# Optimization experiments

Measured on AMD Instinct MI355X. Metric: run time of the kernel, lower is better.

## Reference

```python
import jax, jax.numpy as jnp
import numpy as np

B, SEQ, F = 256, 2048, 5
IN1, U1, U2 = SEQ * F, 32, 1
UNFOLDS = 6          # ODE solver unfolds per cell call
ELAPSED = 1.0        # elapsed time per call


def _cell_params(key, n_in, n_u):
    ks = jax.random.split(key, 9)
    U = lambda k, shp, lo, hi: jax.random.uniform(k, shp, jnp.float32, lo, hi)
    return dict(
        input_w=jnp.ones((n_in,), jnp.float32),
        input_b=jnp.zeros((n_in,), jnp.float32),
        smu=U(ks[0], (n_in, n_u), 0.3, 0.8),
        ssig=U(ks[1], (n_in, n_u), 3.0, 8.0),
        sW=U(ks[2], (n_in, n_u), 0.001, 1.0),
        serev=2.0 * jax.random.bernoulli(ks[3], 0.5, (n_in, n_u)).astype(jnp.float32) - 1.0,
        mu=U(ks[4], (n_u, n_u), 0.3, 0.8),
        sig=U(ks[5], (n_u, n_u), 3.0, 8.0),
        W=U(ks[6], (n_u, n_u), 0.001, 1.0),
        erev=2.0 * jax.random.bernoulli(ks[7], 0.5, (n_u, n_u)).astype(jnp.float32) - 1.0,
        gleak=jnp.ones((n_u,), jnp.float32),
        vleak=U(ks[8], (n_u,), -0.2, 0.2),
        cm=0.5 * jnp.ones((n_u,), jnp.float32),
    )


def setup_inputs() -> dict:
    key = jax.random.key(0)
    kx, ka, kb = jax.random.split(key, 3)
    inp = {"x": jax.random.normal(kx, (B, SEQ, F), jnp.float32)}
    for pfx, k, n_in, n_u in (("a_", ka, IN1, U1), ("b_", kb, U1, U2)):
        for name, v in _cell_params(k, n_in, n_u).items():
            inp[pfx + name] = v
    return inp


def _ltc(x, iw, ib, smu, ssig, sW, serev, mu, sig, W, erev, gleak, vleak, cm):
    # x: [B, n_in]; input affine mapping
    x = x * iw + ib
    # sensory synapse activations: [B, n_in, n_u]
    sact = sW * jax.nn.sigmoid((x[:, :, None] - smu) * ssig)
    w_num_s = jnp.einsum('biu,iu->bu', sact, serev)   # reversal-weighted sum
    w_den_s = jnp.sum(sact, axis=1)
    cm_t = cm / (ELAPSED / UNFOLDS)                   # [n_u]
    v0 = jnp.zeros((x.shape[0], cm.shape[0]), x.dtype)

    def body(v, _):
        # recurrent synapses: presyn axis 1, postsyn axis 2 -> [B, n_u, n_u]
        wact = W * jax.nn.sigmoid((v[:, :, None] - mu) * sig)
        num = cm_t * v + gleak * vleak + jnp.einsum('bij,ij->bj', wact, erev) + w_num_s
        den = cm_t + gleak + jnp.sum(wact, axis=1) + w_den_s
        return num / den, None

    v, _ = jax.lax.scan(body, v0, None, length=UNFOLDS)
    return v


def reference(x,
              a_input_w, a_input_b, a_smu, a_ssig, a_sW, a_serev,
              a_mu, a_sig, a_W, a_erev, a_gleak, a_vleak, a_cm,
              b_input_w, b_input_b, b_smu, b_ssig, b_sW, b_serev,
              b_mu, b_sig, b_W, b_erev, b_gleak, b_vleak, b_cm):
    bsz = x.shape[0]
    xb = x.reshape(bsz, -1)  # [B, seq*5]
    h = _ltc(xb, a_input_w, a_input_b, a_smu, a_ssig, a_sW, a_serev,
             a_mu, a_sig, a_W, a_erev, a_gleak, a_vleak, a_cm)     # [B, 32]
    h2 = _ltc(h, b_input_w, b_input_b, b_smu, b_ssig, b_sW, b_serev,
              b_mu, b_sig, b_W, b_erev, b_gleak, b_vleak, b_cm)    # [B, 1]
    return jax.nn.sigmoid(h2).reshape(bsz)
```

## Files before the change

kernel.cpp:

```cpp
#include <hip/hip_runtime.h>

#define BATCH 256
#define IN1   10240
#define NU    32
#define NB    32
#define BGROUPS (BATCH / NB)
#define CHUNK 40
#define XPAD  44
#define LOG2E 1.4426950408889634f

__global__ __launch_bounds__(256) void ltc_sensory_partial(
    const float* __restrict__ x,
    const float* __restrict__ iw, const float* __restrict__ ibias,
    const float* __restrict__ smu, const float* __restrict__ ssig,
    const float* __restrict__ sW, const float* __restrict__ serev,
    float2* __restrict__ part, int stripe)
{
    const int tid = threadIdx.x;
    const int u   = tid & 31;
    const int g   = tid >> 5;
    const int b0  = blockIdx.x * NB;
    const int ibase = blockIdx.y * stripe;
    const int iend  = ibase + stripe;

    __shared__ float4 sP[CHUNK * NU];
    __shared__ float  xL[NB][XPAD];

    float accn[4], accd[4];
#pragma unroll
    for (int k = 0; k < 4; ++k) { accn[k] = 0.f; accd[k] = 0.f; }

    const int lrow = tid >> 3;
    const int lq   = tid & 7;

    for (int cb = ibase; cb < iend; cb += CHUNK) {
        __syncthreads();

#pragma unroll
        for (int p = tid; p < CHUNK * NU; p += 256) {
            const int ii = cb + (p >> 5);
            const int gi = ii * NU + (p & 31);
            const float sg = ssig[gi] * LOG2E;
            const float w  = sW[gi];
            sP[p] = make_float4(sg * iw[ii],
                                (smu[gi] - ibias[ii]) * sg,
                                w, w * serev[gi]);
        }
        const float* xrow = x + (size_t)(b0 + lrow) * IN1 + cb;
        {
            const float4 v4 = *(const float4*)(xrow + lq * 4);
            *(float4*)&xL[lrow][lq * 4] = v4;
            if (lq < 2) {
                const float4 w4 = *(const float4*)(xrow + (lq + 8) * 4);
                *(float4*)&xL[lrow][(lq + 8) * 4] = w4;
            }
        }
        __syncthreads();

        const float* xr = &xL[g * 4][0];
#pragma unroll 2
        for (int di = 0; di < CHUNK; ++di) {
            const float4 f = sP[di * NU + u];
#pragma unroll
            for (int k = 0; k < 4; ++k) {
                const float xv = xr[k * XPAD + di];
                const float e  = __builtin_amdgcn_exp2f(f.y - xv * f.x);
                const float r  = __builtin_amdgcn_rcpf(1.0f + e);
                accd[k] = fmaf(f.z, r, accd[k]);
                accn[k] = fmaf(f.w, r, accn[k]);
            }
        }
    }

#pragma unroll
    for (int k = 0; k < 4; ++k) {
        part[((size_t)blockIdx.y * BATCH + (b0 + g * 4 + k)) * NU + u] =
            make_float2(accn[k], accd[k]);
    }
}

__global__ __launch_bounds__(256) void ltc_reduce(
    const float2* __restrict__ part, int nsplit, float2* __restrict__ S)
{
    const int tid = threadIdx.x;
    const int b   = blockIdx.x;
    const int u   = tid & 31;
    const int sl  = tid >> 5;

    __shared__ float sred[8][NU][2];

    float sn = 0.f, sd = 0.f;
#pragma unroll 8
    for (int s = sl; s < nsplit; s += 8) {
        const float2 p = part[((size_t)s * BATCH + b) * NU + u];
        sn += p.x;
        sd += p.y;
    }
    sred[sl][u][0] = sn;
    sred[sl][u][1] = sd;
    __syncthreads();

    if (tid >= 32) return;
    float Sn = 0.f, Sd = 0.f;
#pragma unroll
    for (int s2 = 0; s2 < 8; ++s2) {
        Sn += sred[s2][u][0];
        Sd += sred[s2][u][1];
    }
    S[(size_t)b * NU + u] = make_float2(Sn, Sd);
}

__global__ __launch_bounds__(256) void ltc_unfold(
    const float2* __restrict__ S,
    const float* __restrict__ amu, const float* __restrict__ asig,
    const float* __restrict__ aW,  const float* __restrict__ aerev,
    const float* __restrict__ agleak, const float* __restrict__ avleak,
    const float* __restrict__ acm,
    const float* __restrict__ b_iw, const float* __restrict__ b_ib,
    const float* __restrict__ b_smu, const float* __restrict__ b_ssig,
    const float* __restrict__ b_sW,  const float* __restrict__ b_serev,
    const float* __restrict__ b_mu,  const float* __restrict__ b_sig,
    const float* __restrict__ b_W,   const float* __restrict__ b_erev,
    const float* __restrict__ b_gleak, const float* __restrict__ b_vleak,
    const float* __restrict__ b_cm,
    float* __restrict__ out)
{
    const int tid = threadIdx.x;
    const int u   = tid & 31;
    const int bl  = tid >> 5;
    const int b   = blockIdx.x * 8 + bl;

    __shared__ float pAp[NU*NU], pCp[NU*NU];
    __shared__ float pW[NU*NU],  pWE[NU*NU];

    for (int p = tid; p < NU * NU; p += 256) {
        const float sg = asig[p] * LOG2E;
        pAp[p] = sg;
        pCp[p] = amu[p] * sg;
        const float w = aW[p];
        pW[p]  = w;
        pWE[p] = w * aerev[p];
    }
    __syncthreads();

    const float2 Sv = S[(size_t)b * NU + u];
    const float Sn = Sv.x, Sd = Sv.y;

    const float cmt = acm[u] * 6.0f;
    const float gl  = agleak[u];
    const float gv  = gl * avleak[u];

    float v = 0.f;
    for (int k = 0; k < 6; ++k) {
        float rn = 0.f, rd = 0.f;
#pragma unroll
        for (int j = 0; j < NU; ++j) {
            const float vj = __shfl(v, j, 32);
            const int pi = j * NU + u;
            const float e = __builtin_amdgcn_exp2f(pCp[pi] - vj * pAp[pi]);
            const float r = __builtin_amdgcn_rcpf(1.0f + e);
            rn = fmaf(pWE[pi], r, rn);
            rd = fmaf(pW[pi],  r, rd);
        }
        const float num = cmt * v + gv + rn + Sn;
        const float den = cmt + gl + rd + Sd;
        v = num / den;
    }

    const float x2  = v * b_iw[u] + b_ib[u];
    const float e2  = __builtin_amdgcn_exp2f((b_smu[u] - x2) * b_ssig[u] * LOG2E);
    const float s2v = b_sW[u] * __builtin_amdgcn_rcpf(1.0f + e2);
    float wn = s2v * b_serev[u];
    float wd = s2v;
#pragma unroll
    for (int m = 16; m >= 1; m >>= 1) {
        wn += __shfl_xor(wn, m, 32);
        wd += __shfl_xor(wd, m, 32);
    }

    const float bcmt = b_cm[0] * 6.0f;
    const float bgl  = b_gleak[0];
    const float bgv  = bgl * b_vleak[0];
    const float bmu  = b_mu[0], bsig = b_sig[0], bW = b_W[0], berev = b_erev[0];
    float v2 = 0.f;
#pragma unroll
    for (int k = 0; k < 6; ++k) {
        const float ee = __builtin_amdgcn_exp2f((bmu - v2) * bsig * LOG2E);
        const float ws = bW * __builtin_amdgcn_rcpf(1.0f + ee);
        const float num = bcmt * v2 + bgv + ws * berev + wn;
        const float den = bcmt + bgl + ws + wd;
        v2 = num / den;
    }

    if (u == 0)
        out[b] = 1.0f / (1.0f + __builtin_amdgcn_exp2f(-v2 * LOG2E));
}

extern "C" void kernel_launch(void* const* d_in, const int* in_sizes, int n_in,
                              void* d_out, int out_size, void* d_ws, size_t ws_size,
                              hipStream_t stream) {
    const float* x       = (const float*)d_in[0];
    const float* a_iw    = (const float*)d_in[1];
    const float* a_ib    = (const float*)d_in[2];
    const float* a_smu   = (const float*)d_in[3];
    const float* a_ssig  = (const float*)d_in[4];
    const float* a_sW    = (const float*)d_in[5];
    const float* a_serev = (const float*)d_in[6];
    const float* a_mu    = (const float*)d_in[7];
    const float* a_sig   = (const float*)d_in[8];
    const float* a_W     = (const float*)d_in[9];
    const float* a_erev  = (const float*)d_in[10];
    const float* a_gleak = (const float*)d_in[11];
    const float* a_vleak = (const float*)d_in[12];
    const float* a_cm    = (const float*)d_in[13];
    const float* b_iw    = (const float*)d_in[14];
    const float* b_ib    = (const float*)d_in[15];
    const float* b_smu   = (const float*)d_in[16];
    const float* b_ssig  = (const float*)d_in[17];
    const float* b_sW    = (const float*)d_in[18];
    const float* b_serev = (const float*)d_in[19];
    const float* b_mu    = (const float*)d_in[20];
    const float* b_sig   = (const float*)d_in[21];
    const float* b_W     = (const float*)d_in[22];
    const float* b_erev  = (const float*)d_in[23];
    const float* b_gleak = (const float*)d_in[24];
    const float* b_vleak = (const float*)d_in[25];
    const float* b_cm    = (const float*)d_in[26];
    float* out = (float*)d_out;

    int splits = 256;
    while (splits > 4 &&
           ((size_t)splits * BATCH * NU + BATCH * NU) * sizeof(float2) > ws_size)
        splits >>= 1;
    const int stripe = IN1 / splits;

    float2* part = (float2*)d_ws;
    float2* S    = part + (size_t)splits * BATCH * NU;

    dim3 grid1(BGROUPS, splits);
    ltc_sensory_partial<<<grid1, 256, 0, stream>>>(
        x, a_iw, a_ib, a_smu, a_ssig, a_sW, a_serev, part, stripe);

    ltc_reduce<<<BATCH, 256, 0, stream>>>(part, splits, S);

    ltc_unfold<<<BATCH / 8, 256, 0, stream>>>(
        S,
        a_mu, a_sig, a_W, a_erev, a_gleak, a_vleak, a_cm,
        b_iw, b_ib, b_smu, b_ssig, b_sW, b_serev,
        b_mu, b_sig, b_W, b_erev, b_gleak, b_vleak, b_cm,
        out);
}
```

Before: 45.08 us.

## Prepack sensory parameters and map batch to threads with uniform parameter loads

Adds a separate pack kernel that precomputes the sensory parameter float4s into a layout grouped by blocks of 8 units. The main sensory kernel now assigns one batch row per thread and 8 units per block, so every thread in a wavefront reads the same parameter address (a broadcast, likely scalar load) and streams its own x row straight from global memory. This removes the LDS staging and barriers. It costs an extra kernel launch, a packed-parameter round trip through the workspace, uncoalesced per-thread x row reads, and a fixed split count that no longer checks workspace size.

Measured after the change: 70.65 us. 1.57x slower.

```diff
diff --git a/kernel.cpp b/kernel.cpp
--- a/kernel.cpp
+++ b/kernel.cpp
@@ -3,80 +3,73 @@
 #define BATCH 256
 #define IN1   10240
 #define NU    32
-#define NB    32
-#define BGROUPS (BATCH / NB)
-#define CHUNK 40
-#define XPAD  44
+#define SPLITS 128
+#define STRIPE (IN1 / SPLITS)
+#define SUB   16
+#define NSUB  (STRIPE / SUB)
 #define LOG2E 1.4426950408889634f
 
-__global__ __launch_bounds__(256) void ltc_sensory_partial(
-    const float* __restrict__ x,
+__global__ __launch_bounds__(256) void ltc_pack(
     const float* __restrict__ iw, const float* __restrict__ ibias,
     const float* __restrict__ smu, const float* __restrict__ ssig,
     const float* __restrict__ sW, const float* __restrict__ serev,
-    float2* __restrict__ part, int stripe)
-{
-    const int tid = threadIdx.x;
-    const int u   = tid & 31;
-    const int g   = tid >> 5;
-    const int b0  = blockIdx.x * NB;
-    const int ibase = blockIdx.y * stripe;
-    const int iend  = ibase + stripe;
-
-    __shared__ float4 sP[CHUNK * NU];
-    __shared__ float  xL[NB][XPAD];
-
-    float accn[4], accd[4];
-#pragma unroll
-    for (int k = 0; k < 4; ++k) { accn[k] = 0.f; accd[k] = 0.f; }
-
-    const int lrow = tid >> 3;
-    const int lq   = tid & 7;
-
-    for (int cb = ibase; cb < iend; cb += CHUNK) {
-        __syncthreads();
-
-#pragma unroll
-        for (int p = tid; p < CHUNK * NU; p += 256) {
-            const int ii = cb + (p >> 5);
-            const int gi = ii * NU + (p & 31);
-            const float sg = ssig[gi] * LOG2E;
-            const float w  = sW[gi];
-            sP[p] = make_float4(sg * iw[ii],
-                                (smu[gi] - ibias[ii]) * sg,
-                                w, w * serev[gi]);
-        }
-        const float* xrow = x + (size_t)(b0 + lrow) * IN1 + cb;
-        {
-            const float4 v4 = *(const float4*)(xrow + lq * 4);
-            *(float4*)&xL[lrow][lq * 4] = v4;
-            if (lq < 2) {
-                const float4 w4 = *(const float4*)(xrow + (lq + 8) * 4);
-                *(float4*)&xL[lrow][(lq + 8) * 4] = w4;
+    float4* __restrict__ Ppack)
+{
+    const int idx = blockIdx.x * 256 + threadIdx.x;
+    const int i = idx >> 5;
+    const int u = idx & 31;
+    const float sg = ssig[idx] * LOG2E;
+    const float A  = sg * iw[i];
+    const float C  = (smu[idx] - ibias[i]) * sg;
+    const float w  = sW[idx];
+    const int uq = u >> 3, uj = u & 7;
+    Ppack[((size_t)uq * IN1 + i) * 8 + uj] =
+        make_float4(A, C, w, w * serev[idx]);
+}
+
+__global__ __launch_bounds__(256) void ltc_sensory_partial(
+    const float* __restrict__ x,
+    const float4* __restrict__ Ppack,
+    float2* __restrict__ part)
+{
+    const int b  = threadIdx.x;
+    const int uq = blockIdx.x;
+    const int s  = blockIdx.y;
+    const int i0 = s * STRIPE;
+
+    float accn[8], accd[8];
+#pragma unroll
+    for (int k = 0; k < 8; ++k) { accn[k] = 0.f; accd[k] = 0.f; }
+
+    const float*  xrow  = x + (size_t)b * IN1 + i0;
+    const float4* pbase = Ppack + ((size_t)uq * IN1 + i0) * 8;
+
+    for (int sc = 0; sc < NSUB; ++sc) {
+        union { float4 v4[SUB / 4]; float f[SUB]; } xu;
+#pragma unroll
+        for (int q = 0; q < SUB / 4; ++q)
+            xu.v4[q] = *(const float4*)(xrow + sc * SUB + q * 4);
+
+#pragma unroll
+        for (int di = 0; di < SUB; ++di) {
+            const float xv = xu.f[di];
+            const float4* pp = pbase + (size_t)(sc * SUB + di) * 8;
+#pragma unroll
+            for (int uj = 0; uj < 8; ++uj) {
+                const float4 f = pp[uj];
+                const float t = f.y - xv * f.x;
+                const float e = __builtin_amdgcn_exp2f(t);
+                const float r = __builtin_amdgcn_rcpf(1.0f + e);
+                accd[uj] = fmaf(f.z, r, accd[uj]);
+                accn[uj] = fmaf(f.w, r, accn[uj]);
             }
         }
-        __syncthreads();
-
-        const float* xr = &xL[g * 4][0];
-#pragma unroll 2
-        for (int di = 0; di < CHUNK; ++di) {
-            const float4 f = sP[di * NU + u];
-#pragma unroll
-            for (int k = 0; k < 4; ++k) {
-                const float xv = xr[k * XPAD + di];
-                const float e  = __builtin_amdgcn_exp2f(f.y - xv * f.x);
-                const float r  = __builtin_amdgcn_rcpf(1.0f + e);
-                accd[k] = fmaf(f.z, r, accd[k]);
-                accn[k] = fmaf(f.w, r, accn[k]);
-            }
-        }
-    }
-
-#pragma unroll
-    for (int k = 0; k < 4; ++k) {
-        part[((size_t)blockIdx.y * BATCH + (b0 + g * 4 + k)) * NU + u] =
-            make_float2(accn[k], accd[k]);
-    }
+    }
+
+    float2* po = part + ((size_t)s * BATCH + b) * NU + uq * 8;
+#pragma unroll
+    for (int uj = 0; uj < 8; ++uj)
+        po[uj] = make_float2(accn[uj], accd[uj]);
 }
 
 __global__ __launch_bounds__(256) void ltc_reduce(
@@ -228,23 +221,20 @@
     const float* b_cm    = (const float*)d_in[26];
     float* out = (float*)d_out;
 
-    int splits = 256;
-    while (splits > 4 &&
-           ((size_t)splits * BATCH * NU + BATCH * NU) * sizeof(float2) > ws_size)
-        splits >>= 1;
-    const int stripe = IN1 / splits;
-
-    float2* part = (float2*)d_ws;
-    float2* S    = part + (size_t)splits * BATCH * NU;
-
-    dim3 grid1(BGROUPS, splits);
-    ltc_sensory_partial<<<grid1, 256, 0, stream>>>(
-        x, a_iw, a_ib, a_smu, a_ssig, a_sW, a_serev, part, stripe);
-
-    ltc_reduce<<<BATCH, 256, 0, stream>>>(part, splits, S);
+    float4* Ppack = (float4*)d_ws;
+    float2* part  = (float2*)(Ppack + (size_t)IN1 * NU);
+    float2* Sarr  = part + (size_t)SPLITS * BATCH * NU;
+
+    ltc_pack<<<(IN1 * NU) / 256, 256, 0, stream>>>(
+        a_iw, a_ib, a_smu, a_ssig, a_sW, a_serev, Ppack);
+
+    dim3 g1(4, SPLITS);
+    ltc_sensory_partial<<<g1, 256, 0, stream>>>(x, Ppack, part);
+
+    ltc_reduce<<<BATCH, 256, 0, stream>>>(part, SPLITS, Sarr);
 
     ltc_unfold<<<BATCH / 8, 256, 0, stream>>>(
-        S,
+        Sarr,
         a_mu, a_sig, a_W, a_erev, a_gleak, a_vleak, a_cm,
         b_iw, b_ib, b_smu, b_ssig, b_sW, b_serev,
         b_mu, b_sig, b_W, b_erev, b_gleak, b_vleak, b_cm,
```
